# Optimization experiments

Hardware: AMD Instinct MI355X
Metric: run time of the kernel (lower is better)

The kernel has to match this reference:

```python
import jax, jax.numpy as jnp
import numpy as np

D_MODEL, H, G = 2048, 32, 8
D_K = D_MODEL // H          # 64
GROUP_SIZE = H // G         # 4
B, S = 2, 2048


def setup_inputs() -> dict:
    key = jax.random.key(0)
    ks = jax.random.split(key, 9)
    sd = 1.0 / np.sqrt(D_MODEL)
    x = jax.random.normal(ks[0], (B, S, D_MODEL), dtype=jnp.float32)
    Wq = jax.random.normal(ks[1], (D_MODEL, D_MODEL), dtype=jnp.float32) * sd
    bq = jax.random.normal(ks[2], (D_MODEL,), dtype=jnp.float32) * 0.01
    Wk = jax.random.normal(ks[3], (D_MODEL, G * D_K), dtype=jnp.float32) * sd
    bk = jax.random.normal(ks[4], (G * D_K,), dtype=jnp.float32) * 0.01
    Wv = jax.random.normal(ks[5], (D_MODEL, G * D_K), dtype=jnp.float32) * sd
    bv = jax.random.normal(ks[6], (G * D_K,), dtype=jnp.float32) * 0.01
    Wo = jax.random.normal(ks[7], (D_MODEL, D_MODEL), dtype=jnp.float32) * sd
    bo = jax.random.normal(ks[8], (D_MODEL,), dtype=jnp.float32) * 0.01
    return {"x": x, "Wq": Wq, "bq": bq, "Wk": Wk, "bk": bk,
            "Wv": Wv, "bv": bv, "Wo": Wo, "bo": bo}


def reference(x, Wq, bq, Wk, bk, Wv, bv, Wo, bo):
    Bsz, Sln, _ = x.shape
    # projections
    Q = (x @ Wq + bq).reshape(Bsz, Sln, H, D_K).transpose(0, 2, 1, 3)   # [B,h,S,dk]
    K = (x @ Wk + bk).reshape(Bsz, Sln, G, D_K).transpose(0, 2, 1, 3)   # [B,g,S,dk]
    V = (x @ Wv + bv).reshape(Bsz, Sln, G, D_K).transpose(0, 2, 1, 3)   # [B,g,S,dk]
    # reshape Q into groups: [B, g, group_size, S, dk]; K/V broadcast over group dim
    Qg = Q.reshape(Bsz, G, GROUP_SIZE, Sln, D_K)
    scores = jnp.einsum('bgmqd,bgkd->bgmqk', Qg, K) / jnp.sqrt(jnp.float32(D_K))
    attn = jax.nn.softmax(scores, axis=-1)                              # [B,g,gs,S,S]
    out = jnp.einsum('bgmqk,bgkd->bgmqd', attn, V)                      # [B,g,gs,S,dk]
    out = out.reshape(Bsz, H, Sln, D_K).transpose(0, 2, 1, 3).reshape(Bsz, Sln, D_MODEL)
    return out @ Wo + bo
```

## Files before the change

### kernel.cpp

```cpp
#include <hip/hip_runtime.h>
#include <stdint.h>

#define DMODEL 2048
#define NHEADS 32
#define NGRP 8
#define DKH 64
#define BATCH 2
#define SEQ 2048
#define MTOT (BATCH*SEQ)

typedef unsigned short u16;
typedef __bf16 bf16x8 __attribute__((ext_vector_type(8)));
typedef float f32x4 __attribute__((ext_vector_type(4)));

#define QSCALE 0.18033688011112042f

__device__ __forceinline__ u16 f2bf(float f){
    uint32_t x = __float_as_uint(f);
    x += 0x7FFFu + ((x >> 16) & 1u);
    return (u16)(x >> 16);
}

__device__ __forceinline__ u16 f2bf_hw(float f){
    __bf16 h = (__bf16)f;
    return __builtin_bit_cast(u16, h);
}

__device__ __forceinline__ void gld_lds16(const u16* g, u16* l){
    __builtin_amdgcn_global_load_lds(
        (const __attribute__((address_space(1))) uint32_t*)g,
        (__attribute__((address_space(3))) uint32_t*)l, 16, 0, 0);
}


__global__ void cvt_x_kern(const float* __restrict__ x, u16* __restrict__ xb){
    int i = (blockIdx.x * 256 + threadIdx.x) * 4;
    float4 v = *(const float4*)(x + i);
    uint32_t lo = (uint32_t)f2bf(v.x) | ((uint32_t)f2bf(v.y) << 16);
    uint32_t hi = (uint32_t)f2bf(v.z) | ((uint32_t)f2bf(v.w) << 16);
    *(uint2*)(xb + i) = make_uint2(lo, hi);
}

__global__ void cvt_wT_all(const float* __restrict__ Wq, const float* __restrict__ Wk,
                           const float* __restrict__ Wv, const float* __restrict__ Wo,
                           u16* __restrict__ WqT, u16* __restrict__ WkT,
                           u16* __restrict__ WvT, u16* __restrict__ WoT){
    __shared__ float t[32][33];
    int bx = blockIdx.x;
    const float* W; u16* T; int N; int cx;
    if (bx < 64)      { W = Wq; T = WqT; N = 2048; cx = bx; }
    else if (bx < 80) { W = Wk; T = WkT; N = 512;  cx = bx - 64; }
    else if (bx < 96) { W = Wv; T = WvT; N = 512;  cx = bx - 80; }
    else              { W = Wo; T = WoT; N = 2048; cx = bx - 96; }
    int tx = threadIdx.x & 31, ty = threadIdx.x >> 5;
    int n0 = cx * 32, k0 = blockIdx.y * 32;
#pragma unroll
    for (int i = 0; i < 4; i++)
        t[ty*4+i][tx] = W[(size_t)(k0 + ty*4 + i) * N + n0 + tx];
    __syncthreads();
#pragma unroll
    for (int i = 0; i < 4; i++)
        T[(size_t)(n0 + ty*4 + i) * DMODEL + k0 + tx] = f2bf(t[tx][ty*4+i]);
}

template<int EPI>
__global__ __launch_bounds__(256, 2) void gemm_nt(
    const u16* __restrict__ A, const u16* __restrict__ Bt,
    const float* __restrict__ bias0, const float* __restrict__ bias1, const float* __restrict__ bias2,
    void* __restrict__ out0, void* __restrict__ out1, void* __restrict__ out2, int Kn)
{
    __shared__ alignas(16) u16 As[128*32];
    __shared__ alignas(16) u16 Bs[128*32];
    const int tid  = threadIdx.x;
    const int w    = tid >> 6, lane = tid & 63, quad = lane >> 4, l16 = lane & 15;
    const int wr   = w >> 1,  wc   = w & 1;
    const int m0   = blockIdx.x * 128, n0 = blockIdx.y * 128;
    const int arow = lane >> 2, acol = (lane & 3) * 8;

    const u16* ga = A  + (size_t)(m0 + w*32 + arow) * Kn + acol;
    const u16* gb = Bt + (size_t)(n0 + w*32 + arow) * Kn + acol;
    u16* la = As + (w*32) * 32;
    u16* lb = Bs + (w*32) * 32;

    f32x4 acc[4][4] = {};

    for (int k0 = 0; k0 < Kn; k0 += 32){
        __syncthreads();
        gld_lds16(ga + k0,                  la);
        gld_lds16(ga + k0 + (size_t)16*Kn,  la + 16*32);
        gld_lds16(gb + k0,                  lb);
        gld_lds16(gb + k0 + (size_t)16*Kn,  lb + 16*32);
        __syncthreads();
        bf16x8 af[4], bfr[4];
#pragma unroll
        for (int t = 0; t < 4; t++)
            af[t]  = *(const bf16x8*)(As + (wr*64 + t*16 + l16)*32 + quad*8);
#pragma unroll
        for (int t = 0; t < 4; t++)
            bfr[t] = *(const bf16x8*)(Bs + (wc*64 + t*16 + l16)*32 + quad*8);
#pragma unroll
        for (int tm = 0; tm < 4; tm++)
#pragma unroll
            for (int tn = 0; tn < 4; tn++)
                acc[tm][tn] = __builtin_amdgcn_mfma_f32_16x16x32_bf16(af[tm], bfr[tn], acc[tm][tn], 0, 0, 0);
    }

#pragma unroll
    for (int tn = 0; tn < 4; tn++){
        int col = n0 + wc*64 + tn*16 + l16;
        float bv;
        if (EPI == 3) bv = (col < 2048) ? bias0[col] : (col < 2560) ? bias1[col-2048] : bias2[col-2560];
        else          bv = bias0[col];
#pragma unroll
        for (int tm = 0; tm < 4; tm++){
#pragma unroll
            for (int r = 0; r < 4; r++){
                int row = m0 + wr*64 + tm*16 + quad*4 + r;
                float v = acc[tm][tn][r] + bv;
                if (EPI == 3){
                    int b = row >> 11, s = row & (SEQ-1);
                    if (col < 2048){
                        int hh = col >> 6, d = col & 63;
                        ((u16*)out0)[(((size_t)b*NHEADS + hh)*SEQ + s)*DKH + d] = f2bf(v * QSCALE);
                    } else if (col < 2560){
                        int c = col - 2048, gg = c >> 6, d = c & 63;
                        ((u16*)out1)[(((size_t)b*NGRP + gg)*SEQ + s)*DKH + d] = f2bf(v);
                    } else {
                        int c = col - 2560, gg = c >> 6, d = c & 63;
                        ((u16*)out2)[(((size_t)b*NGRP + gg)*DKH + d)*SEQ + s] = f2bf(v);
                    }
                } else {
                    ((float*)out0)[(size_t)row * DMODEL + col] = v;
                }
            }
        }
    }
}

#define PSTR 76
__global__ __launch_bounds__(256, 2) void flash_kern(
    const u16* __restrict__ Qb, const u16* __restrict__ Kb,
    const u16* __restrict__ Vt, u16* __restrict__ Ob)
{
    __shared__ alignas(16) u16 Ks[2][64*64];
    __shared__ alignas(16) u16 Vs[2][64*64];
    __shared__ alignas(16) u16 Ps[256*PSTR];
    const int tid = threadIdx.x, w = tid >> 6, lane = tid & 63;
    const int quad = lane >> 4, l16 = lane & 15;
    const int q0 = blockIdx.x * 256;
    const int h  = blockIdx.y, b = blockIdx.z, g = h >> 2;

    const u16* Qg = Qb + (((size_t)b*NHEADS + h)*SEQ + q0 + w*64) * DKH;
    const u16* Kg = Kb + ((size_t)b*NGRP + g) * SEQ * DKH;
    const u16* Vg = Vt + ((size_t)b*NGRP + g) * DKH * SEQ;

    const int lr = lane >> 3, lc = lane & 7;
    const int sw = lc ^ (lr & 7);
    const u16* gk0 = Kg + (size_t)(w*16 + lr) * DKH + sw*8;
    const u16* gk1 = gk0 + (size_t)8 * DKH;
    const u16* gv0 = Vg + (size_t)(w*16 + lr) * SEQ + sw*8;
    const u16* gv1 = gv0 + (size_t)8 * SEQ;

    bf16x8 aq[2][4];
#pragma unroll
    for (int tm = 0; tm < 4; tm++)
#pragma unroll
        for (int ks = 0; ks < 2; ks++)
            aq[ks][tm] = *(const bf16x8*)(Qg + (tm*16 + l16)*DKH + ks*32 + quad*8);

    float lsum[4][4] = {};
    f32x4 oa[4][4] = {};

#define STAGE(buf, kt) do{                                            \
        u16* lk = Ks[buf] + (w*16)*64;                                \
        u16* lv = Vs[buf] + (w*16)*64;                                \
        gld_lds16(gk0 + (size_t)(kt)*64*DKH, lk);                     \
        gld_lds16(gk1 + (size_t)(kt)*64*DKH, lk + 8*64);              \
        gld_lds16(gv0 + (size_t)(kt)*64,     lv);                     \
        gld_lds16(gv1 + (size_t)(kt)*64,     lv + 8*64);              \
    }while(0)

#define COMPUTE(buf) do{                                                              \
        f32x4 sa[4][4] = {};                                                          \
        _Pragma("unroll")                                                             \
        for (int tn = 0; tn < 4; tn++){                                               \
            _Pragma("unroll")                                                         \
            for (int ks = 0; ks < 2; ks++){                                           \
                bf16x8 bk = *(const bf16x8*)(Ks[buf] + (tn*16 + l16)*64               \
                                             + (((ks*4+quad) ^ (l16&7)) * 8));        \
                _Pragma("unroll")                                                     \
                for (int tm = 0; tm < 4; tm++)                                        \
                    sa[tm][tn] = __builtin_amdgcn_mfma_f32_16x16x32_bf16(             \
                        aq[ks][tm], bk, sa[tm][tn], 0, 0, 0);                         \
            }                                                                         \
        }                                                                             \
        _Pragma("unroll")                                                             \
        for (int tm = 0; tm < 4; tm++)                                                \
            _Pragma("unroll")                                                         \
            for (int tn = 0; tn < 4; tn++)                                            \
                _Pragma("unroll")                                                     \
                for (int r = 0; r < 4; r++){                                          \
                    float p = __builtin_amdgcn_exp2f(sa[tm][tn][r]);                  \
                    lsum[tm][r] += p;                                                 \
                    Ps[(w*64 + tm*16 + quad*4 + r)*PSTR + tn*16 + l16] = f2bf_hw(p);  \
                }                                                                     \
        _Pragma("unroll")                                                             \
        for (int ks = 0; ks < 2; ks++){                                               \
            bf16x8 ap[4];                                                             \
            _Pragma("unroll")                                                         \
            for (int tm = 0; tm < 4; tm++)                                            \
                ap[tm] = *(const bf16x8*)(Ps + (w*64 + tm*16 + l16)*PSTR              \
                                          + ks*32 + quad*8);                          \
            _Pragma("unroll")                                                         \
            for (int tn = 0; tn < 4; tn++){                                           \
                bf16x8 bv8 = *(const bf16x8*)(Vs[buf] + (tn*16 + l16)*64              \
                                              + (((ks*4+quad) ^ (l16&7)) * 8));       \
                _Pragma("unroll")                                                     \
                for (int tm = 0; tm < 4; tm++)                                        \
                    oa[tm][tn] = __builtin_amdgcn_mfma_f32_16x16x32_bf16(             \
                        ap[tm], bv8, oa[tm][tn], 0, 0, 0);                            \
            }                                                                         \
        }                                                                             \
    }while(0)

    STAGE(0, 0);
    __syncthreads();

    for (int kt2 = 0; kt2 < SEQ/128; ++kt2){
        int kt = kt2 * 2;
        STAGE(1, kt + 1);
        COMPUTE(0);
        __syncthreads();
        if (kt2 < SEQ/128 - 1) STAGE(0, kt + 2);
        COMPUTE(1);
        __syncthreads();
    }

#pragma unroll
    for (int tm = 0; tm < 4; tm++)
#pragma unroll
        for (int r = 0; r < 4; r++){
            float s = lsum[tm][r];
#pragma unroll
            for (int d = 1; d < 16; d <<= 1) s += __shfl_xor(s, d, 64);
            lsum[tm][r] = 1.0f / s;
        }

#pragma unroll
    for (int tm = 0; tm < 4; tm++)
#pragma unroll
        for (int r = 0; r < 4; r++){
            int q = q0 + w*64 + tm*16 + quad*4 + r;
            float inv = lsum[tm][r];
#pragma unroll
            for (int tn = 0; tn < 4; tn++)
                Ob[((size_t)b*SEQ + q)*DMODEL + h*DKH + tn*16 + l16] = f2bf(oa[tm][tn][r] * inv);
        }
#undef STAGE
#undef COMPUTE
}


extern "C" void kernel_launch(void* const* d_in, const int* in_sizes, int n_in,
                              void* d_out, int out_size, void* d_ws, size_t ws_size,
                              hipStream_t stream)
{
    const float* x  = (const float*)d_in[0];
    const float* Wq = (const float*)d_in[1];
    const float* bq = (const float*)d_in[2];
    const float* Wk = (const float*)d_in[3];
    const float* bk = (const float*)d_in[4];
    const float* Wv = (const float*)d_in[5];
    const float* bv = (const float*)d_in[6];
    const float* Wo = (const float*)d_in[7];
    const float* bo = (const float*)d_in[8];

    uint8_t* p = (uint8_t*)d_ws;
    u16* xb  = (u16*)p; p += (size_t)MTOT*DMODEL*2;
    u16* WqT = (u16*)p; p += (size_t)DMODEL*DMODEL*2;
    u16* WkT = (u16*)p; p += (size_t)(NGRP*DKH)*DMODEL*2;
    u16* WvT = (u16*)p; p += (size_t)(NGRP*DKH)*DMODEL*2;
    u16* WoT = (u16*)p; p += (size_t)DMODEL*DMODEL*2;
    u16* Qb  = (u16*)p; p += (size_t)BATCH*NHEADS*SEQ*DKH*2;
    u16* Kb  = (u16*)p; p += (size_t)BATCH*NGRP*SEQ*DKH*2;
    u16* Vtb = (u16*)p; p += (size_t)BATCH*NGRP*DKH*SEQ*2;
    u16* Ob  = (u16*)p; p += (size_t)MTOT*DMODEL*2;

    cvt_x_kern<<<MTOT*DMODEL/1024, 256, 0, stream>>>(x, xb);
    cvt_wT_all<<<dim3(160, 64), 256, 0, stream>>>(Wq, Wk, Wv, Wo, WqT, WkT, WvT, WoT);

    gemm_nt<3><<<dim3(MTOT/128, 3072/128), 256, 0, stream>>>(
        xb, WqT, bq, bk, bv, Qb, Kb, Vtb, DMODEL);

    flash_kern<<<dim3(SEQ/256, NHEADS, BATCH), 256, 0, stream>>>(Qb, Kb, Vtb, Ob);

    gemm_nt<2><<<dim3(MTOT/128, DMODEL/128), 256, 0, stream>>>(
        Ob, WoT, bo, nullptr, nullptr, d_out, nullptr, nullptr, DMODEL);
}
```

Baseline: 322.7 us.

## Restructure flash attention to 8 waves of 32 query rows with transposed scores

The attention kernel now launches 512 threads (8 waves), each handling 32 query rows instead of 64, which roughly halves per-wave accumulator registers and raises the launch bound to 4 blocks. The QK^T MFMA operands are swapped so each lane holds four consecutive key scores for one query row. This lets P be written to LDS as packed 64-bit stores, and row sums reduce with two shuffles instead of four. K/V staging is split across more waves with one load each. The gain in occupancy and latency hiding comes at the cost of less Q-fragment reuse per K/V LDS read and more LDS traffic per FLOP.

Result: slower. 452.2 us (+40.1%).

```diff
diff --git a/kernel.cpp b/kernel.cpp
--- a/kernel.cpp
+++ b/kernel.cpp
@@ -24,6 +24,10 @@
 __device__ __forceinline__ u16 f2bf_hw(float f){
     __bf16 h = (__bf16)f;
     return __builtin_bit_cast(u16, h);
+}
+
+__device__ __forceinline__ uint32_t pk2bf(float a, float b){
+    return (uint32_t)f2bf_hw(a) | ((uint32_t)f2bf_hw(b) << 16);
 }
 
 __device__ __forceinline__ void gld_lds16(const u16* g, u16* l){
@@ -137,88 +141,84 @@
     }
 }
 
-#define PSTR 76
-__global__ __launch_bounds__(256, 2) void flash_kern(
+#define KD 72
+__global__ __launch_bounds__(512, 4) void flash_kern(
     const u16* __restrict__ Qb, const u16* __restrict__ Kb,
     const u16* __restrict__ Vt, u16* __restrict__ Ob)
 {
     __shared__ alignas(16) u16 Ks[2][64*64];
     __shared__ alignas(16) u16 Vs[2][64*64];
-    __shared__ alignas(16) u16 Ps[256*PSTR];
+    __shared__ alignas(16) u16 Ps[256*KD];
     const int tid = threadIdx.x, w = tid >> 6, lane = tid & 63;
     const int quad = lane >> 4, l16 = lane & 15;
     const int q0 = blockIdx.x * 256;
     const int h  = blockIdx.y, b = blockIdx.z, g = h >> 2;
 
-    const u16* Qg = Qb + (((size_t)b*NHEADS + h)*SEQ + q0 + w*64) * DKH;
+    const u16* Qg = Qb + (((size_t)b*NHEADS + h)*SEQ + q0 + w*32) * DKH;
     const u16* Kg = Kb + ((size_t)b*NGRP + g) * SEQ * DKH;
     const u16* Vg = Vt + ((size_t)b*NGRP + g) * DKH * SEQ;
 
     const int lr = lane >> 3, lc = lane & 7;
-    const int sw = lc ^ (lr & 7);
-    const u16* gk0 = Kg + (size_t)(w*16 + lr) * DKH + sw*8;
-    const u16* gk1 = gk0 + (size_t)8 * DKH;
-    const u16* gv0 = Vg + (size_t)(w*16 + lr) * SEQ + sw*8;
-    const u16* gv1 = gv0 + (size_t)8 * SEQ;
-
-    bf16x8 aq[2][4];
-#pragma unroll
-    for (int tm = 0; tm < 4; tm++)
+    const int sw = lc ^ lr;
+    const u16* gk0 = Kg + (size_t)(w*8 + lr) * DKH + sw*8;
+    const u16* gv0 = Vg + (size_t)(w*8 + lr) * SEQ + sw*8;
+
+    bf16x8 aq[2][2];
+#pragma unroll
+    for (int nt = 0; nt < 2; nt++)
 #pragma unroll
         for (int ks = 0; ks < 2; ks++)
-            aq[ks][tm] = *(const bf16x8*)(Qg + (tm*16 + l16)*DKH + ks*32 + quad*8);
-
-    float lsum[4][4] = {};
-    f32x4 oa[4][4] = {};
+            aq[ks][nt] = *(const bf16x8*)(Qg + (nt*16 + l16)*DKH + ks*32 + quad*8);
+
+    float lsum[2] = {0.f, 0.f};
+    f32x4 oa[2][4] = {};
 
 #define STAGE(buf, kt) do{                                            \
-        u16* lk = Ks[buf] + (w*16)*64;                                \
-        u16* lv = Vs[buf] + (w*16)*64;                                \
-        gld_lds16(gk0 + (size_t)(kt)*64*DKH, lk);                     \
-        gld_lds16(gk1 + (size_t)(kt)*64*DKH, lk + 8*64);              \
-        gld_lds16(gv0 + (size_t)(kt)*64,     lv);                     \
-        gld_lds16(gv1 + (size_t)(kt)*64,     lv + 8*64);              \
+        gld_lds16(gk0 + (size_t)(kt)*64*DKH, Ks[buf] + (w*8)*64);     \
+        gld_lds16(gv0 + (size_t)(kt)*64,     Vs[buf] + (w*8)*64);     \
     }while(0)
 
 #define COMPUTE(buf) do{                                                              \
-        f32x4 sa[4][4] = {};                                                          \
+        f32x4 sa[4][2] = {};                                                          \
         _Pragma("unroll")                                                             \
-        for (int tn = 0; tn < 4; tn++){                                               \
+        for (int ks = 0; ks < 2; ks++){                                               \
             _Pragma("unroll")                                                         \
-            for (int ks = 0; ks < 2; ks++){                                           \
-                bf16x8 bk = *(const bf16x8*)(Ks[buf] + (tn*16 + l16)*64               \
+            for (int kt = 0; kt < 4; kt++){                                           \
+                bf16x8 bk = *(const bf16x8*)(Ks[buf] + (kt*16 + l16)*64               \
                                              + (((ks*4+quad) ^ (l16&7)) * 8));        \
-                _Pragma("unroll")                                                     \
-                for (int tm = 0; tm < 4; tm++)                                        \
-                    sa[tm][tn] = __builtin_amdgcn_mfma_f32_16x16x32_bf16(             \
-                        aq[ks][tm], bk, sa[tm][tn], 0, 0, 0);                         \
+                sa[kt][0] = __builtin_amdgcn_mfma_f32_16x16x32_bf16(                  \
+                    bk, aq[ks][0], sa[kt][0], 0, 0, 0);                               \
+                sa[kt][1] = __builtin_amdgcn_mfma_f32_16x16x32_bf16(                  \
+                    bk, aq[ks][1], sa[kt][1], 0, 0, 0);                               \
             }                                                                         \
         }                                                                             \
         _Pragma("unroll")                                                             \
-        for (int tm = 0; tm < 4; tm++)                                                \
+        for (int nt = 0; nt < 2; nt++){                                               \
+            float ls = 0.f;                                                           \
             _Pragma("unroll")                                                         \
-            for (int tn = 0; tn < 4; tn++)                                            \
-                _Pragma("unroll")                                                     \
-                for (int r = 0; r < 4; r++){                                          \
-                    float p = __builtin_amdgcn_exp2f(sa[tm][tn][r]);                  \
-                    lsum[tm][r] += p;                                                 \
-                    Ps[(w*64 + tm*16 + quad*4 + r)*PSTR + tn*16 + l16] = f2bf_hw(p);  \
-                }                                                                     \
+            for (int kt = 0; kt < 4; kt++){                                           \
+                float e0 = __builtin_amdgcn_exp2f(sa[kt][nt][0]);                     \
+                float e1 = __builtin_amdgcn_exp2f(sa[kt][nt][1]);                     \
+                float e2 = __builtin_amdgcn_exp2f(sa[kt][nt][2]);                     \
+                float e3 = __builtin_amdgcn_exp2f(sa[kt][nt][3]);                     \
+                ls += (e0 + e1) + (e2 + e3);                                          \
+                uint2 pk = make_uint2(pk2bf(e0, e1), pk2bf(e2, e3));                  \
+                *(uint2*)(Ps + (w*32 + nt*16 + l16)*KD + kt*16 + quad*4) = pk;        \
+            }                                                                         \
+            lsum[nt] += ls;                                                           \
+        }                                                                             \
         _Pragma("unroll")                                                             \
         for (int ks = 0; ks < 2; ks++){                                               \
-            bf16x8 ap[4];                                                             \
-            _Pragma("unroll")                                                         \
-            for (int tm = 0; tm < 4; tm++)                                            \
-                ap[tm] = *(const bf16x8*)(Ps + (w*64 + tm*16 + l16)*PSTR              \
-                                          + ks*32 + quad*8);                          \
+            bf16x8 ap0 = *(const bf16x8*)(Ps + (w*32 +  0 + l16)*KD + ks*32 + quad*8);\
+            bf16x8 ap1 = *(const bf16x8*)(Ps + (w*32 + 16 + l16)*KD + ks*32 + quad*8);\
             _Pragma("unroll")                                                         \
             for (int tn = 0; tn < 4; tn++){                                           \
                 bf16x8 bv8 = *(const bf16x8*)(Vs[buf] + (tn*16 + l16)*64              \
                                               + (((ks*4+quad) ^ (l16&7)) * 8));       \
-                _Pragma("unroll")                                                     \
-                for (int tm = 0; tm < 4; tm++)                                        \
-                    oa[tm][tn] = __builtin_amdgcn_mfma_f32_16x16x32_bf16(             \
-                        ap[tm], bv8, oa[tm][tn], 0, 0, 0);                            \
+                oa[0][tn] = __builtin_amdgcn_mfma_f32_16x16x32_bf16(                  \
+                    ap0, bv8, oa[0][tn], 0, 0, 0);                                    \
+                oa[1][tn] = __builtin_amdgcn_mfma_f32_16x16x32_bf16(                  \
+                    ap1, bv8, oa[1][tn], 0, 0, 0);                                    \
             }                                                                         \
         }                                                                             \
     }while(0)
@@ -237,21 +237,19 @@
     }
 
 #pragma unroll
-    for (int tm = 0; tm < 4; tm++)
+    for (int nt = 0; nt < 2; nt++){
+        float s = lsum[nt];
+        s += __shfl_xor(s, 16, 64);
+        s += __shfl_xor(s, 32, 64);
+        lsum[nt] = 1.0f / s;
+    }
+
+#pragma unroll
+    for (int tm = 0; tm < 2; tm++)
 #pragma unroll
         for (int r = 0; r < 4; r++){
-            float s = lsum[tm][r];
-#pragma unroll
-            for (int d = 1; d < 16; d <<= 1) s += __shfl_xor(s, d, 64);
-            lsum[tm][r] = 1.0f / s;
-        }
-
-#pragma unroll
-    for (int tm = 0; tm < 4; tm++)
-#pragma unroll
-        for (int r = 0; r < 4; r++){
-            int q = q0 + w*64 + tm*16 + quad*4 + r;
-            float inv = lsum[tm][r];
+            float inv = __shfl(lsum[tm], quad*4 + r, 64);
+            int q = q0 + w*32 + tm*16 + quad*4 + r;
 #pragma unroll
             for (int tn = 0; tn < 4; tn++)
                 Ob[((size_t)b*SEQ + q)*DMODEL + h*DKH + tn*16 + l16] = f2bf(oa[tm][tn][r] * inv);
@@ -292,7 +290,7 @@
     gemm_nt<3><<<dim3(MTOT/128, 3072/128), 256, 0, stream>>>(
         xb, WqT, bq, bk, bv, Qb, Kb, Vtb, DMODEL);
 
-    flash_kern<<<dim3(SEQ/256, NHEADS, BATCH), 256, 0, stream>>>(Qb, Kb, Vtb, Ob);
+    flash_kern<<<dim3(SEQ/256, NHEADS, BATCH), 512, 0, stream>>>(Qb, Kb, Vtb, Ob);
 
     gemm_nt<2><<<dim3(MTOT/128, DMODEL/128), 256, 0, stream>>>(
         Ob, WoT, bo, nullptr, nullptr, d_out, nullptr, nullptr, DMODEL);
```
